# Performance work log

Measured on AMD Instinct MI355X. Metric: run time of the kernel, lower is better.

Reference implementation:

```python
import jax, jax.numpy as jnp
import numpy as np

B, C, H, W = 32, 512, 32, 32
HEADS = 8
HD = C // HEADS  # 64
BN_EPS = 1e-5


def setup_inputs() -> dict:
    key = jax.random.key(0)
    ks = jax.random.split(key, 8)
    s = 0.02  # trunc_normal std for Linear weights
    x = jax.random.normal(ks[0], (B, C, H, W), jnp.float32)
    Wq = jax.random.normal(ks[1], (C, C), jnp.float32) * s
    Wk = jax.random.normal(ks[2], (C, C), jnp.float32) * s
    Wv = jax.random.normal(ks[3], (C, C), jnp.float32) * s
    # depthwise 3x3 kernel, kaiming fan_out (fan_out = 3*3*1 per group)
    dw_w = jax.random.normal(ks[4], (C, 1, 3, 3), jnp.float32) * np.sqrt(2.0 / 9.0)
    bn_gamma = jnp.ones((C,), jnp.float32)
    bn_beta = jnp.zeros((C,), jnp.float32)
    temperature = jnp.ones((HEADS, 1, 1), jnp.float32)
    Wp = jax.random.normal(ks[5], (C, C), jnp.float32) * s
    bp = jnp.zeros((C,), jnp.float32)
    return {"x": x, "Wq": Wq, "Wk": Wk, "Wv": Wv, "dw_w": dw_w,
            "bn_gamma": bn_gamma, "bn_beta": bn_beta,
            "temperature": temperature, "Wp": Wp, "bp": bp}


def _l2norm(t):
    # torch F.normalize: x / max(||x||, eps)
    n = jnp.sqrt(jnp.sum(t * t, axis=-1, keepdims=True))
    return t / jnp.maximum(n, 1e-12)


def _forward(x, Wq, Wk, Wv, dw_w, bn_gamma, bn_beta, temperature, Wp, bp):
    b, c, h, w = x.shape
    n = h * w
    x_flat = x.transpose(0, 2, 3, 1).reshape(b, n, c)  # [B,N,C]

    q = (x_flat @ Wq.T).reshape(b, n, HEADS, HD).transpose(0, 2, 3, 1)  # [B,h,d,N]
    k = (x_flat @ Wk.T).reshape(b, n, HEADS, HD).transpose(0, 2, 3, 1)
    q = _l2norm(q)
    k = _l2norm(k)

    attn = jnp.einsum('bhdn,bhen->bhde', q, k) * temperature  # [B,h,d,d]
    attn = jax.nn.softmax(attn, axis=-1)

    v_content = x_flat @ Wv.T  # [B,N,C]

    # gated value path: DWConv -> BatchNorm (batch stats, train mode) -> SiLU
    g = jax.lax.conv_general_dilated(
        x, dw_w, window_strides=(1, 1), padding=((1, 1), (1, 1)),
        feature_group_count=c, dimension_numbers=('NCHW', 'OIHW', 'NCHW'))
    mu = jnp.mean(g, axis=(0, 2, 3), keepdims=True)
    var = jnp.var(g, axis=(0, 2, 3), keepdims=True)
    g = (g - mu) * jax.lax.rsqrt(var + BN_EPS)
    g = g * bn_gamma[None, :, None, None] + bn_beta[None, :, None, None]
    g = g * jax.nn.sigmoid(g)  # SiLU
    v_gate = g.transpose(0, 2, 3, 1).reshape(b, n, c)

    v = (v_content * v_gate).reshape(b, n, HEADS, HD).transpose(0, 2, 3, 1)  # [B,h,d,N]
    out = jnp.einsum('bhde,bhen->bhdn', attn, v)  # [B,h,d,N]
    out = out.transpose(0, 3, 1, 2).reshape(b, n, c)  # [B,N,C]
    out = out @ Wp.T + bp
    return out.reshape(b, h, w, c).transpose(0, 3, 1, 2)  # [B,C,H,W]


def reference(x, Wq, Wk, Wv, dw_w, bn_gamma, bn_beta, temperature, Wp, bp):
    return _forward(x, Wq, Wk, Wv, dw_w, bn_gamma, bn_beta, temperature, Wp, bp)
```

## Files before the change

kernel.cpp:

```cpp
#include <hip/hip_runtime.h>
#include <stdint.h>

#define BATCH 32
#define CCH   512
#define NPIX  1024
#define HEADS 8
#define QKV_M 1536

typedef short bf16x8 __attribute__((ext_vector_type(8)));
typedef float f32x4 __attribute__((ext_vector_type(4)));
typedef unsigned short u16x8 __attribute__((ext_vector_type(8)));

__device__ inline float bf2f(unsigned short u) {
  union { float f; uint32_t i; } t; t.i = ((uint32_t)u) << 16; return t.f;
}
__device__ inline unsigned short f2bf(float f) {
  union { float f; uint32_t u; } t; t.f = f;
  uint32_t u = t.u;
  return (unsigned short)((u + 0x7FFFu + ((u >> 16) & 1u)) >> 16);
}

__device__ inline void gl_lds16(const unsigned short* g, unsigned short* l) {
  __builtin_amdgcn_global_load_lds(
      (const __attribute__((address_space(1))) uint32_t*)g,
      (__attribute__((address_space(3))) uint32_t*)l, 16, 0, 0);
}

__global__ void convert_w(const float* __restrict__ Wq, const float* __restrict__ Wk,
                          const float* __restrict__ Wv, const float* __restrict__ Wp,
                          unsigned short* __restrict__ wcat,
                          unsigned short* __restrict__ wpb) {
  int i = (blockIdx.x * 256 + threadIdx.x) * 4;
  union { ushort4 u4; unsigned short s[4]; } o;
  f32x4 a;
  a = *(const f32x4*)&Wq[i];
  for (int j = 0; j < 4; j++) o.s[j] = f2bf(a[j]);
  *(ushort4*)&wcat[i] = o.u4;
  a = *(const f32x4*)&Wk[i];
  for (int j = 0; j < 4; j++) o.s[j] = f2bf(a[j]);
  *(ushort4*)&wcat[CCH * CCH + i] = o.u4;
  a = *(const f32x4*)&Wv[i];
  for (int j = 0; j < 4; j++) o.s[j] = f2bf(a[j]);
  *(ushort4*)&wcat[2 * CCH * CCH + i] = o.u4;
  a = *(const f32x4*)&Wp[i];
  for (int j = 0; j < 4; j++) o.s[j] = f2bf(a[j]);
  *(ushort4*)&wpb[i] = o.u4;
}

__global__ void transpose_f2b(const float* __restrict__ in,
                              unsigned short* __restrict__ out) {
  __shared__ float tile[64][65];
  const int b  = blockIdx.z;
  const int p0 = blockIdx.x * 64;
  const int c0 = blockIdx.y * 64;
  const float* inb = in + (size_t)b * CCH * NPIX;
  unsigned short* outb = out + (size_t)b * NPIX * CCH;
  const int t = threadIdx.x;
  const int cr = t >> 2, tl = t & 3;
#pragma unroll
  for (int j = 0; j < 4; ++j) {
    const int off = j * 16 + tl * 4;
    f32x4 v = *(const f32x4*)&inb[(size_t)(c0 + cr) * NPIX + p0 + off];
    tile[cr][off + 0] = v[0];
    tile[cr][off + 1] = v[1];
    tile[cr][off + 2] = v[2];
    tile[cr][off + 3] = v[3];
  }
  __syncthreads();
  const int pr = t >> 3, cc = (t & 7) * 8;
#pragma unroll
  for (int pass = 0; pass < 2; ++pass) {
    const int p = pr + pass * 32;
    union { u16x8 v; unsigned short s[8]; } o;
#pragma unroll
    for (int j = 0; j < 8; ++j) o.s[j] = f2bf(tile[cc + j][p]);
    *(u16x8*)&outb[(size_t)(p0 + p) * CCH + c0 + cc] = o.v;
  }
}

template <bool OUT_F32>
__launch_bounds__(512, 2)
__global__ void gemm_bt(const unsigned short* __restrict__ A,
                        const unsigned short* __restrict__ X,
                        void* __restrict__ Cout,
                        const float* __restrict__ bias,
                        int M, int N, int K) {
  __shared__ __align__(16) unsigned short As[2][256 * 64];
  __shared__ __align__(16) unsigned short Bs[2][256 * 64];
  const int b  = blockIdx.z;
  const int m0 = blockIdx.y * 256;
  const int n0 = blockIdx.x * 256;
  const unsigned short* Xb = X + (size_t)b * N * K;
  const int tid  = threadIdx.x;
  const int lane = tid & 63;
  const int wave = tid >> 6;
  const int wm = wave >> 2;
  const int wn = wave & 3;
  const int quad = lane >> 4, l16 = lane & 15;

  f32x4 acc[8][4];
  const f32x4 zero = {0.f, 0.f, 0.f, 0.f};
#pragma unroll
  for (int i = 0; i < 8; i++)
#pragma unroll
    for (int j = 0; j < 4; j++) acc[i][j] = zero;

  const int r8  = lane >> 3;
  const int swk = ((lane & 7) ^ r8) * 8;
  const unsigned short* Ag = A  + (size_t)(m0 + wave * 32 + r8) * K + swk;
  const unsigned short* Xg = Xb + (size_t)(n0 + wave * 32 + r8) * K + swk;

  const int NT = K >> 6;

  auto stage = [&](int kt, int bsel) {
    unsigned short* Al = &As[bsel][wave * 32 * 64];
    unsigned short* Bl = &Bs[bsel][wave * 32 * 64];
    const unsigned short* Agk = Ag + kt * 64;
    const unsigned short* Xgk = Xg + kt * 64;
#pragma unroll
    for (int i = 0; i < 4; ++i) {
      gl_lds16(Agk + (size_t)i * 8 * K, Al + i * 8 * 64);
      gl_lds16(Xgk + (size_t)i * 8 * K, Bl + i * 8 * 64);
    }
  };

  stage(0, 0);
  if (NT > 1) stage(1, 1);
  asm volatile("s_waitcnt vmcnt(8)" ::: "memory");
  __builtin_amdgcn_s_barrier();

  for (int t = 0; t < NT; ++t) {
    const int cur = t & 1;
    const unsigned short* Asl = As[cur];
    const unsigned short* Bsl = Bs[cur];

    {
      bf16x8 a0[8], b0[4];
      const int ch0 = ((0 * 4 + quad) ^ (l16 & 7)) * 8;
#pragma unroll
      for (int ii = 0; ii < 8; ++ii)
        a0[ii] = *(const bf16x8*)&Asl[(wm * 128 + ii * 16 + l16) * 64 + ch0];
#pragma unroll
      for (int jj = 0; jj < 4; ++jj)
        b0[jj] = *(const bf16x8*)&Bsl[(wn * 64 + jj * 16 + l16) * 64 + ch0];

      bf16x8 a1[8], b1[4];
      const int ch1 = ((1 * 4 + quad) ^ (l16 & 7)) * 8;
#pragma unroll
      for (int ii = 0; ii < 8; ++ii)
        a1[ii] = *(const bf16x8*)&Asl[(wm * 128 + ii * 16 + l16) * 64 + ch1];
#pragma unroll
      for (int jj = 0; jj < 4; ++jj)
        b1[jj] = *(const bf16x8*)&Bsl[(wn * 64 + jj * 16 + l16) * 64 + ch1];

#pragma unroll
      for (int ii = 0; ii < 8; ++ii)
#pragma unroll
        for (int jj = 0; jj < 4; ++jj)
          acc[ii][jj] = __builtin_amdgcn_mfma_f32_16x16x32_bf16(
              a0[ii], b0[jj], acc[ii][jj], 0, 0, 0);
#pragma unroll
      for (int ii = 0; ii < 8; ++ii)
#pragma unroll
        for (int jj = 0; jj < 4; ++jj)
          acc[ii][jj] = __builtin_amdgcn_mfma_f32_16x16x32_bf16(
              a1[ii], b1[jj], acc[ii][jj], 0, 0, 0);
    }

    __builtin_amdgcn_s_barrier();
    if (t + 2 < NT) {
      stage(t + 2, cur);
      asm volatile("s_waitcnt vmcnt(8)" ::: "memory");
    } else if (t + 1 < NT) {
      asm volatile("s_waitcnt vmcnt(0)" ::: "memory");
    }
    __builtin_amdgcn_s_barrier();
  }

#pragma unroll
  for (int i = 0; i < 8; ++i) {
#pragma unroll
    for (int r = 0; r < 4; ++r) {
      const int gm = m0 + wm * 128 + i * 16 + quad * 4 + r;
      if constexpr (OUT_F32) {
        const float bv = bias[gm];
        float* Co = (float*)Cout + (size_t)b * M * N + (size_t)gm * N +
                    n0 + wn * 64 + l16;
#pragma unroll
        for (int j = 0; j < 4; ++j) Co[j * 16] = acc[i][j][r] + bv;
      } else {
        unsigned short* Co = (unsigned short*)Cout + (size_t)b * M * N +
                             (size_t)gm * N + n0 + wn * 64 + l16;
#pragma unroll
        for (int j = 0; j < 4; ++j) Co[j * 16] = f2bf(acc[i][j][r]);
      }
    }
  }
}

__global__ void dw_stats(const float* __restrict__ x,
                         const float* __restrict__ wgt,
                         float* __restrict__ s1, float* __restrict__ s2) {
  int c = blockIdx.x, b = blockIdx.y;
  __shared__ __align__(16) float plane[NPIX];
  const float* xp = x + ((size_t)b * CCH + c) * NPIX;
  *(f32x4*)&plane[threadIdx.x * 4] = *(const f32x4*)&xp[threadIdx.x * 4];
  __syncthreads();
  float w[9];
  for (int i = 0; i < 9; i++) w[i] = wgt[c * 9 + i];
  float a1 = 0.f, a2 = 0.f;
  for (int pi = 0; pi < 4; pi++) {
    int p = threadIdx.x + pi * 256;
    int h = p >> 5, wc = p & 31;
    float v = 0.f;
    for (int dh = -1; dh <= 1; dh++)
      for (int dw = -1; dw <= 1; dw++) {
        int hh = h + dh, ww = wc + dw;
        if (hh >= 0 && hh < 32 && ww >= 0 && ww < 32)
          v += w[(dh + 1) * 3 + dw + 1] * plane[hh * 32 + ww];
      }
    a1 += v; a2 += v * v;
  }
  for (int off = 32; off > 0; off >>= 1) {
    a1 += __shfl_down(a1, off);
    a2 += __shfl_down(a2, off);
  }
  __shared__ float r1[4], r2[4];
  int wv = threadIdx.x >> 6;
  if ((threadIdx.x & 63) == 0) { r1[wv] = a1; r2[wv] = a2; }
  __syncthreads();
  if (threadIdx.x == 0) {
    atomicAdd(&s1[c], r1[0] + r1[1] + r1[2] + r1[3]);
    atomicAdd(&s2[c], r2[0] + r2[1] + r2[2] + r2[3]);
  }
}

__global__ void gate_apply(const float* __restrict__ x,
                           const float* __restrict__ wgt,
                           const float* __restrict__ s1, const float* __restrict__ s2,
                           const float* __restrict__ gamma,
                           const float* __restrict__ beta,
                           unsigned short* __restrict__ qkv) {
  int c = blockIdx.x, b = blockIdx.y;
  __shared__ __align__(16) float plane[NPIX];
  const float* xp = x + ((size_t)b * CCH + c) * NPIX;
  *(f32x4*)&plane[threadIdx.x * 4] = *(const f32x4*)&xp[threadIdx.x * 4];
  __syncthreads();
  float w[9];
  for (int i = 0; i < 9; i++) w[i] = wgt[c * 9 + i];
  const float invn = 1.f / 32768.f;
  float mean = s1[c] * invn;
  float var = fmaxf(s2[c] * invn - mean * mean, 0.f);
  float rstd = rsqrtf(var + 1e-5f);
  float ga = gamma[c], be = beta[c];

  const int t = threadIdx.x;
  const int h = t >> 3, w0 = (t & 7) * 4;
  unsigned short* vp = qkv + ((size_t)b * QKV_M + 2 * CCH + c) * NPIX + h * 32 + w0;
  union { ushort4 q; unsigned short s[4]; } vv;
  vv.q = *(const ushort4*)vp;
#pragma unroll
  for (int i = 0; i < 4; ++i) {
    const int wc = w0 + i;
    float val = 0.f;
    for (int dh = -1; dh <= 1; dh++)
      for (int dw = -1; dw <= 1; dw++) {
        int hh = h + dh, ww = wc + dw;
        if (hh >= 0 && hh < 32 && ww >= 0 && ww < 32)
          val += w[(dh + 1) * 3 + dw + 1] * plane[hh * 32 + ww];
      }
    float g = (val - mean) * rstd * ga + be;
    float sg = g / (1.f + __expf(-g));
    vv.s[i] = f2bf(bf2f(vv.s[i]) * sg);
  }
  *(ushort4*)vp = vv.q;
}

__launch_bounds__(256)
__global__ void attn_s(const unsigned short* __restrict__ qkv,
                       const float* __restrict__ temp,
                       unsigned short* __restrict__ P) {
  int bh = blockIdx.x;
  int b = bh >> 3, h = bh & 7;
  const unsigned short* Q = qkv + ((size_t)b * QKV_M + h * 64) * NPIX;
  const unsigned short* K = Q + (size_t)CCH * NPIX;
  int tid = threadIdx.x, lane = tid & 63, wave = tid >> 6;
  int quad = lane >> 4, l16 = lane & 15;

  __shared__ __align__(16) float Sf[64][65];
  __shared__ float qq[64], kk[64], invq[64], invk[64];
  __shared__ float redm[4][64], reds[4][64];

  f32x4 zero = {0.f, 0.f, 0.f, 0.f};
  f32x4 acc[4], accQ = zero, accK = zero;
  for (int j = 0; j < 4; j++) acc[j] = zero;
  for (int n0 = 0; n0 < NPIX; n0 += 32) {
    bf16x8 a  = *(const bf16x8*)&Q[(size_t)(wave * 16 + l16) * NPIX + n0 + quad * 8];
    bf16x8 ak = *(const bf16x8*)&K[(size_t)(wave * 16 + l16) * NPIX + n0 + quad * 8];
    accQ = __builtin_amdgcn_mfma_f32_16x16x32_bf16(a, a, accQ, 0, 0, 0);
    accK = __builtin_amdgcn_mfma_f32_16x16x32_bf16(ak, ak, accK, 0, 0, 0);
    for (int j = 0; j < 4; j++) {
      bf16x8 bb = *(const bf16x8*)&K[(size_t)(j * 16 + l16) * NPIX + n0 + quad * 8];
      acc[j] = __builtin_amdgcn_mfma_f32_16x16x32_bf16(a, bb, acc[j], 0, 0, 0);
    }
  }
  for (int j = 0; j < 4; j++)
    for (int r = 0; r < 4; r++)
      Sf[wave * 16 + quad * 4 + r][j * 16 + l16] = acc[j][r];
  for (int r = 0; r < 4; r++)
    if (l16 == quad * 4 + r) {
      qq[wave * 16 + l16] = accQ[r];
      kk[wave * 16 + l16] = accK[r];
    }
  __syncthreads();
  if (tid < 64) invq[tid] = 1.f / fmaxf(sqrtf(qq[tid]), 1e-12f);
  else if (tid < 128) invk[tid - 64] = 1.f / fmaxf(sqrtf(kk[tid - 64]), 1e-12f);
  __syncthreads();

  int row = tid & 63, seg = tid >> 6;
  float fq = temp[h] * invq[row];
  float v[16], pm = -1e30f;
  for (int i = 0; i < 16; i++) {
    v[i] = Sf[row][seg * 16 + i] * fq * invk[seg * 16 + i];
    pm = fmaxf(pm, v[i]);
  }
  redm[seg][row] = pm;
  __syncthreads();
  float m = fmaxf(fmaxf(redm[0][row], redm[1][row]),
                  fmaxf(redm[2][row], redm[3][row]));
  float ps = 0.f;
  for (int i = 0; i < 16; i++) { v[i] = __expf(v[i] - m); ps += v[i]; }
  reds[seg][row] = ps;
  __syncthreads();
  float inv = 1.f / (reds[0][row] + reds[1][row] + reds[2][row] + reds[3][row]);
  union { uint4 q4[2]; unsigned short s[16]; } u;
  for (int i = 0; i < 16; i++) u.s[i] = f2bf(v[i] * inv);
  unsigned short* Pp = P + ((size_t)bh * 64 + row) * 64 + seg * 16;
  *(uint4*)&Pp[0] = u.q4[0];
  *(uint4*)&Pp[8] = u.q4[1];
}

__launch_bounds__(256)
__global__ void attn_o(const unsigned short* __restrict__ qkv,
                       const unsigned short* __restrict__ P,
                       unsigned short* __restrict__ aoT) {
  int blk = blockIdx.x;
  int nc = blk & 3, bh = blk >> 2;
  int b = bh >> 3, h = bh & 7;
  const unsigned short* V = qkv + ((size_t)b * QKV_M + 2 * CCH + h * 64) * NPIX;
  unsigned short* Ob = aoT + (size_t)b * NPIX * CCH + h * 64;
  int tid = threadIdx.x, lane = tid & 63, wave = tid >> 6;
  int quad = lane >> 4, l16 = lane & 15;

  __shared__ __align__(16) unsigned short Vt[4][16][72];
  __shared__ __align__(16) unsigned short Ot[4][16][72];

  const unsigned short* Pb = P + (size_t)bh * 64 * 64;
  bf16x8 Pf[4][2];
  for (int j = 0; j < 4; j++)
    for (int ks = 0; ks < 2; ks++)
      Pf[j][ks] = *(const bf16x8*)&Pb[(j * 16 + l16) * 64 + ks * 32 + quad * 8];

  f32x4 zero = {0.f, 0.f, 0.f, 0.f};
  int e1 = lane >> 1, noff = (lane & 1) * 8;
  int nbase = nc * 256 + wave * 64;
  int orow = lane >> 3, ocol = (lane & 7) * 8;

  union { uint4 q; unsigned short s[8]; } g0, g1, c0, c1;
  g0.q = *(const uint4*)&V[(size_t)e1 * NPIX + nbase + noff];
  g1.q = *(const uint4*)&V[(size_t)(e1 + 32) * NPIX + nbase + noff];
#pragma unroll
  for (int nt = 0; nt < 4; nt++) {
    int n0 = nbase + nt * 16;
    c0 = g0; c1 = g1;
    if (nt < 3) {
      g0.q = *(const uint4*)&V[(size_t)e1 * NPIX + n0 + 16 + noff];
      g1.q = *(const uint4*)&V[(size_t)(e1 + 32) * NPIX + n0 + 16 + noff];
    }
    for (int jj = 0; jj < 8; jj++) {
      Vt[wave][noff + jj][e1]      = c0.s[jj];
      Vt[wave][noff + jj][e1 + 32] = c1.s[jj];
    }
    bf16x8 Af0 = *(const bf16x8*)&Vt[wave][l16][quad * 8];
    bf16x8 Af1 = *(const bf16x8*)&Vt[wave][l16][32 + quad * 8];
    f32x4 oacc[4];
    for (int j = 0; j < 4; j++) {
      oacc[j] = __builtin_amdgcn_mfma_f32_16x16x32_bf16(Af0, Pf[j][0], zero, 0, 0, 0);
      oacc[j] = __builtin_amdgcn_mfma_f32_16x16x32_bf16(Af1, Pf[j][1], oacc[j], 0, 0, 0);
    }
    for (int j = 0; j < 4; j++)
      for (int r = 0; r < 4; r++)
        Ot[wave][quad * 4 + r][j * 16 + l16] = f2bf(oacc[j][r]);
    uint4 o0 = *(const uint4*)&Ot[wave][orow][ocol];
    uint4 o1 = *(const uint4*)&Ot[wave][orow + 8][ocol];
    *(uint4*)&Ob[(size_t)(n0 + orow) * CCH + ocol] = o0;
    *(uint4*)&Ob[(size_t)(n0 + orow + 8) * CCH + ocol] = o1;
  }
}

extern "C" void kernel_launch(void* const* d_in, const int* in_sizes, int n_in,
                              void* d_out, int out_size, void* d_ws, size_t ws_size,
                              hipStream_t stream) {
  const float* x     = (const float*)d_in[0];
  const float* Wq    = (const float*)d_in[1];
  const float* Wk    = (const float*)d_in[2];
  const float* Wv    = (const float*)d_in[3];
  const float* dww   = (const float*)d_in[4];
  const float* gamma = (const float*)d_in[5];
  const float* beta  = (const float*)d_in[6];
  const float* temp  = (const float*)d_in[7];
  const float* Wp    = (const float*)d_in[8];
  const float* bp    = (const float*)d_in[9];
  float* out = (float*)d_out;

  char* ws = (char*)d_ws;
  unsigned short* wcat = (unsigned short*)ws;
  unsigned short* wpb  = wcat + (size_t)QKV_M * CCH;
  float* s1 = (float*)(wpb + (size_t)CCH * CCH);
  float* s2 = s1 + CCH;
  unsigned short* Pbuf = (unsigned short*)(s2 + CCH);
  char* dyn = (char*)(Pbuf + (size_t)BATCH * HEADS * 64 * 64);
  size_t fixed = (size_t)(dyn - ws);
  size_t per_b = ((size_t)NPIX * CCH + (size_t)QKV_M * NPIX) * 2;
  int BC = BATCH;
  while (BC > 1 && fixed + (size_t)BC * per_b > ws_size) BC >>= 1;
  unsigned short* xT  = (unsigned short*)dyn;
  unsigned short* qkv = xT + (size_t)BC * NPIX * CCH;

  convert_w<<<CCH * CCH / 1024, 256, 0, stream>>>(Wq, Wk, Wv, Wp, wcat, wpb);
  hipMemsetAsync(s1, 0, 2 * CCH * sizeof(float), stream);
  dw_stats<<<dim3(CCH, BATCH), 256, 0, stream>>>(x, dww, s1, s2);

  for (int b0 = 0; b0 < BATCH; b0 += BC) {
    const float* xc = x + (size_t)b0 * CCH * NPIX;
    float* outc = out + (size_t)b0 * CCH * NPIX;
    transpose_f2b<<<dim3(NPIX / 64, CCH / 64, BC), 256, 0, stream>>>(xc, xT);
    gemm_bt<false><<<dim3(NPIX / 256, QKV_M / 256, BC), 512, 0, stream>>>(
        wcat, xT, qkv, nullptr, QKV_M, NPIX, CCH);
    attn_s<<<BC * HEADS, 256, 0, stream>>>(qkv, temp, Pbuf);
    gate_apply<<<dim3(CCH, BC), 256, 0, stream>>>(xc, dww, s1, s2, gamma, beta, qkv);
    attn_o<<<BC * HEADS * 4, 256, 0, stream>>>(qkv, Pbuf, xT);
    gemm_bt<true><<<dim3(NPIX / 256, CCH / 256, BC), 512, 0, stream>>>(
        wpb, xT, outc, bp, CCH, NPIX, CCH);
  }
}
```

Before: 323.3 us.

## Split attention kernels across more waves and blocks for higher parallelism

attn_s now runs 16 waves per block, each handling a quarter of the pixel dimension. Partial Gram sums and squared norms are reduced through shared memory before the softmax, which is spread over 16 segments per row. attn_o launches twice as many blocks, each covering half the pixels. The aim is to raise occupancy: only 256 blocks of attn_s exist on a GPU with many CUs. The cost is a larger shared-memory footprint and an extra cross-wave reduction step.

```diff
diff --git a/kernel.cpp b/kernel.cpp
--- a/kernel.cpp
+++ b/kernel.cpp
@@ -276,7 +276,7 @@
   *(ushort4*)vp = vv.q;
 }
 
-__launch_bounds__(256)
+__launch_bounds__(1024)
 __global__ void attn_s(const unsigned short* __restrict__ qkv,
                        const float* __restrict__ temp,
                        unsigned short* __restrict__ P) {
@@ -285,59 +285,88 @@
   const unsigned short* Q = qkv + ((size_t)b * QKV_M + h * 64) * NPIX;
   const unsigned short* K = Q + (size_t)CCH * NPIX;
   int tid = threadIdx.x, lane = tid & 63, wave = tid >> 6;
+  int r16 = wave & 3;
+  int ns  = wave >> 2;
   int quad = lane >> 4, l16 = lane & 15;
 
-  __shared__ __align__(16) float Sf[64][65];
-  __shared__ float qq[64], kk[64], invq[64], invk[64];
-  __shared__ float redm[4][64], reds[4][64];
+  __shared__ float Sp[4][64][68];
+  __shared__ float qqp[4][64], kkp[4][64];
+  __shared__ float invq[64], invk[64];
+  __shared__ float redm[16][64], reds[16][64];
 
   f32x4 zero = {0.f, 0.f, 0.f, 0.f};
   f32x4 acc[4], accQ = zero, accK = zero;
+#pragma unroll
   for (int j = 0; j < 4; j++) acc[j] = zero;
-  for (int n0 = 0; n0 < NPIX; n0 += 32) {
-    bf16x8 a  = *(const bf16x8*)&Q[(size_t)(wave * 16 + l16) * NPIX + n0 + quad * 8];
-    bf16x8 ak = *(const bf16x8*)&K[(size_t)(wave * 16 + l16) * NPIX + n0 + quad * 8];
+
+  const int nbase = ns * 256;
+  for (int n0 = nbase; n0 < nbase + 256; n0 += 32) {
+    bf16x8 a  = *(const bf16x8*)&Q[(size_t)(r16 * 16 + l16) * NPIX + n0 + quad * 8];
+    bf16x8 ak = *(const bf16x8*)&K[(size_t)(r16 * 16 + l16) * NPIX + n0 + quad * 8];
     accQ = __builtin_amdgcn_mfma_f32_16x16x32_bf16(a, a, accQ, 0, 0, 0);
     accK = __builtin_amdgcn_mfma_f32_16x16x32_bf16(ak, ak, accK, 0, 0, 0);
+#pragma unroll
     for (int j = 0; j < 4; j++) {
       bf16x8 bb = *(const bf16x8*)&K[(size_t)(j * 16 + l16) * NPIX + n0 + quad * 8];
       acc[j] = __builtin_amdgcn_mfma_f32_16x16x32_bf16(a, bb, acc[j], 0, 0, 0);
     }
   }
+#pragma unroll
   for (int j = 0; j < 4; j++)
+#pragma unroll
     for (int r = 0; r < 4; r++)
-      Sf[wave * 16 + quad * 4 + r][j * 16 + l16] = acc[j][r];
+      Sp[ns][r16 * 16 + quad * 4 + r][j * 16 + l16] = acc[j][r];
+#pragma unroll
   for (int r = 0; r < 4; r++)
     if (l16 == quad * 4 + r) {
-      qq[wave * 16 + l16] = accQ[r];
-      kk[wave * 16 + l16] = accK[r];
-    }
-  __syncthreads();
-  if (tid < 64) invq[tid] = 1.f / fmaxf(sqrtf(qq[tid]), 1e-12f);
-  else if (tid < 128) invk[tid - 64] = 1.f / fmaxf(sqrtf(kk[tid - 64]), 1e-12f);
-  __syncthreads();
-
-  int row = tid & 63, seg = tid >> 6;
+      qqp[ns][r16 * 16 + l16] = accQ[r];
+      kkp[ns][r16 * 16 + l16] = accK[r];
+    }
+  __syncthreads();
+
+  const int row = tid >> 4, c0 = (tid & 15) * 4;
+#pragma unroll
+  for (int i = 0; i < 4; ++i) {
+    float s = Sp[0][row][c0 + i] + Sp[1][row][c0 + i] +
+              Sp[2][row][c0 + i] + Sp[3][row][c0 + i];
+    Sp[0][row][c0 + i] = s;
+  }
+  if (tid < 64) {
+    float q4 = qqp[0][tid] + qqp[1][tid] + qqp[2][tid] + qqp[3][tid];
+    invq[tid] = 1.f / fmaxf(sqrtf(q4), 1e-12f);
+  } else if (tid < 128) {
+    int r = tid - 64;
+    float k4 = kkp[0][r] + kkp[1][r] + kkp[2][r] + kkp[3][r];
+    invk[r] = 1.f / fmaxf(sqrtf(k4), 1e-12f);
+  }
+  __syncthreads();
+
+  const int seg = tid & 15;
   float fq = temp[h] * invq[row];
-  float v[16], pm = -1e30f;
-  for (int i = 0; i < 16; i++) {
-    v[i] = Sf[row][seg * 16 + i] * fq * invk[seg * 16 + i];
+  float v[4], pm = -1e30f;
+#pragma unroll
+  for (int i = 0; i < 4; i++) {
+    v[i] = Sp[0][row][seg * 4 + i] * fq * invk[seg * 4 + i];
     pm = fmaxf(pm, v[i]);
   }
   redm[seg][row] = pm;
   __syncthreads();
-  float m = fmaxf(fmaxf(redm[0][row], redm[1][row]),
-                  fmaxf(redm[2][row], redm[3][row]));
+  float m = -1e30f;
+#pragma unroll
+  for (int s = 0; s < 16; s++) m = fmaxf(m, redm[s][row]);
   float ps = 0.f;
-  for (int i = 0; i < 16; i++) { v[i] = __expf(v[i] - m); ps += v[i]; }
+#pragma unroll
+  for (int i = 0; i < 4; i++) { v[i] = __expf(v[i] - m); ps += v[i]; }
   reds[seg][row] = ps;
   __syncthreads();
-  float inv = 1.f / (reds[0][row] + reds[1][row] + reds[2][row] + reds[3][row]);
-  union { uint4 q4[2]; unsigned short s[16]; } u;
-  for (int i = 0; i < 16; i++) u.s[i] = f2bf(v[i] * inv);
-  unsigned short* Pp = P + ((size_t)bh * 64 + row) * 64 + seg * 16;
-  *(uint4*)&Pp[0] = u.q4[0];
-  *(uint4*)&Pp[8] = u.q4[1];
+  float tot = 0.f;
+#pragma unroll
+  for (int s = 0; s < 16; s++) tot += reds[s][row];
+  float inv = 1.f / tot;
+  union { ushort4 q; unsigned short s[4]; } u;
+#pragma unroll
+  for (int i = 0; i < 4; i++) u.s[i] = f2bf(v[i] * inv);
+  *(ushort4*)&P[((size_t)bh * 64 + row) * 64 + seg * 4] = u.q;
 }
 
 __launch_bounds__(256)
@@ -345,7 +374,7 @@
                        const unsigned short* __restrict__ P,
                        unsigned short* __restrict__ aoT) {
   int blk = blockIdx.x;
-  int nc = blk & 3, bh = blk >> 2;
+  int nc = blk & 7, bh = blk >> 3;
   int b = bh >> 3, h = bh & 7;
   const unsigned short* V = qkv + ((size_t)b * QKV_M + 2 * CCH + h * 64) * NPIX;
   unsigned short* Ob = aoT + (size_t)b * NPIX * CCH + h * 64;
@@ -363,17 +392,17 @@
 
   f32x4 zero = {0.f, 0.f, 0.f, 0.f};
   int e1 = lane >> 1, noff = (lane & 1) * 8;
-  int nbase = nc * 256 + wave * 64;
+  int nbase = nc * 128 + wave * 32;
   int orow = lane >> 3, ocol = (lane & 7) * 8;
 
   union { uint4 q; unsigned short s[8]; } g0, g1, c0, c1;
   g0.q = *(const uint4*)&V[(size_t)e1 * NPIX + nbase + noff];
   g1.q = *(const uint4*)&V[(size_t)(e1 + 32) * NPIX + nbase + noff];
 #pragma unroll
-  for (int nt = 0; nt < 4; nt++) {
+  for (int nt = 0; nt < 2; nt++) {
     int n0 = nbase + nt * 16;
     c0 = g0; c1 = g1;
-    if (nt < 3) {
+    if (nt < 1) {
       g0.q = *(const uint4*)&V[(size_t)e1 * NPIX + n0 + 16 + noff];
       g1.q = *(const uint4*)&V[(size_t)(e1 + 32) * NPIX + n0 + 16 + noff];
     }
@@ -437,9 +466,9 @@
     transpose_f2b<<<dim3(NPIX / 64, CCH / 64, BC), 256, 0, stream>>>(xc, xT);
     gemm_bt<false><<<dim3(NPIX / 256, QKV_M / 256, BC), 512, 0, stream>>>(
         wcat, xT, qkv, nullptr, QKV_M, NPIX, CCH);
-    attn_s<<<BC * HEADS, 256, 0, stream>>>(qkv, temp, Pbuf);
+    attn_s<<<BC * HEADS, 1024, 0, stream>>>(qkv, temp, Pbuf);
     gate_apply<<<dim3(CCH, BC), 256, 0, stream>>>(xc, dww, s1, s2, gamma, beta, qkv);
-    attn_o<<<BC * HEADS * 4, 256, 0, stream>>>(qkv, Pbuf, xT);
+    attn_o<<<BC * HEADS * 8, 256, 0, stream>>>(qkv, Pbuf, xT);
     gemm_bt<true><<<dim3(NPIX / 256, CCH / 256, BC), 512, 0, stream>>>(
         wpb, xT, outc, bp, CCH, NPIX, CCH);
   }
```

Measured after the change: 322.9 us. Within noise of the previous version (-0.1%).

## Merge independent kernels into combined launches and split attn_o finer

Applied to the files above, without the earlier changes.

Folds the stats zeroing into the weight-conversion kernel, replacing hipMemsetAsync. Merges dw_stats with the input transpose, and gate_apply with attn_s, as block-index-dispatched combined kernels so independent work shares a launch and fills the GPU. It also doubles attn_o's grid with half the pixel range per block. The fast path applies only when the whole batch fits in workspace. The legacy chunked path is kept as a fallback, at the cost of more LDS per merged block and mixed workloads in one grid.

```diff
diff --git a/kernel.cpp b/kernel.cpp
--- a/kernel.cpp
+++ b/kernel.cpp
@@ -26,10 +26,16 @@
       (__attribute__((address_space(3))) uint32_t*)l, 16, 0, 0);
 }
 
-__global__ void convert_w(const float* __restrict__ Wq, const float* __restrict__ Wk,
-                          const float* __restrict__ Wv, const float* __restrict__ Wp,
-                          unsigned short* __restrict__ wcat,
-                          unsigned short* __restrict__ wpb) {
+__global__ void prep_w(const float* __restrict__ Wq, const float* __restrict__ Wk,
+                       const float* __restrict__ Wv, const float* __restrict__ Wp,
+                       unsigned short* __restrict__ wcat,
+                       unsigned short* __restrict__ wpb,
+                       float* __restrict__ s1, float* __restrict__ s2) {
+  if (blockIdx.x == 0) {
+    const f32x4 z4 = {0.f, 0.f, 0.f, 0.f};
+    if (threadIdx.x < 128) ((f32x4*)s1)[threadIdx.x] = z4;
+    else ((f32x4*)s2)[threadIdx.x - 128] = z4;
+  }
   int i = (blockIdx.x * 256 + threadIdx.x) * 4;
   union { ushort4 u4; unsigned short s[4]; } o;
   f32x4 a;
@@ -47,14 +53,48 @@
   *(ushort4*)&wpb[i] = o.u4;
 }
 
-__global__ void transpose_f2b(const float* __restrict__ in,
-                              unsigned short* __restrict__ out) {
-  __shared__ float tile[64][65];
-  const int b  = blockIdx.z;
-  const int p0 = blockIdx.x * 64;
-  const int c0 = blockIdx.y * 64;
-  const float* inb = in + (size_t)b * CCH * NPIX;
-  unsigned short* outb = out + (size_t)b * NPIX * CCH;
+
+__device__ __forceinline__ void stats_body(const float* __restrict__ xp,
+                                           const float* __restrict__ wgt, int c,
+                                           float* __restrict__ s1,
+                                           float* __restrict__ s2,
+                                           float* __restrict__ plane,
+                                           float* __restrict__ r1,
+                                           float* __restrict__ r2) {
+  *(f32x4*)&plane[threadIdx.x * 4] = *(const f32x4*)&xp[threadIdx.x * 4];
+  __syncthreads();
+  float w[9];
+  for (int i = 0; i < 9; i++) w[i] = wgt[c * 9 + i];
+  float a1 = 0.f, a2 = 0.f;
+  for (int pi = 0; pi < 4; pi++) {
+    int p = threadIdx.x + pi * 256;
+    int h = p >> 5, wc = p & 31;
+    float v = 0.f;
+    for (int dh = -1; dh <= 1; dh++)
+      for (int dw = -1; dw <= 1; dw++) {
+        int hh = h + dh, ww = wc + dw;
+        if (hh >= 0 && hh < 32 && ww >= 0 && ww < 32)
+          v += w[(dh + 1) * 3 + dw + 1] * plane[hh * 32 + ww];
+      }
+    a1 += v; a2 += v * v;
+  }
+  for (int off = 32; off > 0; off >>= 1) {
+    a1 += __shfl_down(a1, off);
+    a2 += __shfl_down(a2, off);
+  }
+  int wv = threadIdx.x >> 6;
+  if ((threadIdx.x & 63) == 0) { r1[wv] = a1; r2[wv] = a2; }
+  __syncthreads();
+  if (threadIdx.x == 0) {
+    atomicAdd(&s1[c], r1[0] + r1[1] + r1[2] + r1[3]);
+    atomicAdd(&s2[c], r2[0] + r2[1] + r2[2] + r2[3]);
+  }
+}
+
+__device__ __forceinline__ void transpose_body(const float* __restrict__ inb,
+                                               unsigned short* __restrict__ outb,
+                                               int p0, int c0,
+                                               float (*tile)[65]) {
   const int t = threadIdx.x;
   const int cr = t >> 2, tl = t & 3;
 #pragma unroll
@@ -76,6 +116,186 @@
     for (int j = 0; j < 8; ++j) o.s[j] = f2bf(tile[cc + j][p]);
     *(u16x8*)&outb[(size_t)(p0 + p) * CCH + c0 + cc] = o.v;
   }
+}
+
+__device__ __forceinline__ void gate_body(const float* __restrict__ xp,
+                                          const float* __restrict__ wgt, int c,
+                                          const float* __restrict__ s1,
+                                          const float* __restrict__ s2,
+                                          const float* __restrict__ gamma,
+                                          const float* __restrict__ beta,
+                                          unsigned short* __restrict__ vbase,
+                                          float* __restrict__ plane) {
+  *(f32x4*)&plane[threadIdx.x * 4] = *(const f32x4*)&xp[threadIdx.x * 4];
+  __syncthreads();
+  float w[9];
+  for (int i = 0; i < 9; i++) w[i] = wgt[c * 9 + i];
+  const float invn = 1.f / 32768.f;
+  float mean = s1[c] * invn;
+  float var = fmaxf(s2[c] * invn - mean * mean, 0.f);
+  float rstd = rsqrtf(var + 1e-5f);
+  float ga = gamma[c], be = beta[c];
+  const int t = threadIdx.x;
+  const int h = t >> 3, w0 = (t & 7) * 4;
+  unsigned short* vp = vbase + h * 32 + w0;
+  union { ushort4 q; unsigned short s[4]; } vv;
+  vv.q = *(const ushort4*)vp;
+#pragma unroll
+  for (int i = 0; i < 4; ++i) {
+    const int wc = w0 + i;
+    float val = 0.f;
+    for (int dh = -1; dh <= 1; dh++)
+      for (int dw = -1; dw <= 1; dw++) {
+        int hh = h + dh, ww = wc + dw;
+        if (hh >= 0 && hh < 32 && ww >= 0 && ww < 32)
+          val += w[(dh + 1) * 3 + dw + 1] * plane[hh * 32 + ww];
+      }
+    float g = (val - mean) * rstd * ga + be;
+    float sg = g / (1.f + __expf(-g));
+    vv.s[i] = f2bf(bf2f(vv.s[i]) * sg);
+  }
+  *(ushort4*)vp = vv.q;
+}
+
+__device__ __forceinline__ void attn_s_body(const unsigned short* __restrict__ qkv,
+                                            const float* __restrict__ temp,
+                                            unsigned short* __restrict__ P, int bh,
+                                            float (*Sf)[65],
+                                            float* qq, float* kk,
+                                            float* invq, float* invk,
+                                            float (*redm)[64], float (*reds)[64]) {
+  int b = bh >> 3, h = bh & 7;
+  const unsigned short* Q = qkv + ((size_t)b * QKV_M + h * 64) * NPIX;
+  const unsigned short* K = Q + (size_t)CCH * NPIX;
+  int tid = threadIdx.x, lane = tid & 63, wave = tid >> 6;
+  int quad = lane >> 4, l16 = lane & 15;
+
+  f32x4 zero = {0.f, 0.f, 0.f, 0.f};
+  f32x4 acc[4], accQ = zero, accK = zero;
+  for (int j = 0; j < 4; j++) acc[j] = zero;
+  for (int n0 = 0; n0 < NPIX; n0 += 32) {
+    bf16x8 a  = *(const bf16x8*)&Q[(size_t)(wave * 16 + l16) * NPIX + n0 + quad * 8];
+    bf16x8 ak = *(const bf16x8*)&K[(size_t)(wave * 16 + l16) * NPIX + n0 + quad * 8];
+    accQ = __builtin_amdgcn_mfma_f32_16x16x32_bf16(a, a, accQ, 0, 0, 0);
+    accK = __builtin_amdgcn_mfma_f32_16x16x32_bf16(ak, ak, accK, 0, 0, 0);
+    for (int j = 0; j < 4; j++) {
+      bf16x8 bb = *(const bf16x8*)&K[(size_t)(j * 16 + l16) * NPIX + n0 + quad * 8];
+      acc[j] = __builtin_amdgcn_mfma_f32_16x16x32_bf16(a, bb, acc[j], 0, 0, 0);
+    }
+  }
+  for (int j = 0; j < 4; j++)
+    for (int r = 0; r < 4; r++)
+      Sf[wave * 16 + quad * 4 + r][j * 16 + l16] = acc[j][r];
+  for (int r = 0; r < 4; r++)
+    if (l16 == quad * 4 + r) {
+      qq[wave * 16 + l16] = accQ[r];
+      kk[wave * 16 + l16] = accK[r];
+    }
+  __syncthreads();
+  if (tid < 64) invq[tid] = 1.f / fmaxf(sqrtf(qq[tid]), 1e-12f);
+  else if (tid < 128) invk[tid - 64] = 1.f / fmaxf(sqrtf(kk[tid - 64]), 1e-12f);
+  __syncthreads();
+
+  int row = tid & 63, seg = tid >> 6;
+  float fq = temp[h] * invq[row];
+  float v[16], pm = -1e30f;
+  for (int i = 0; i < 16; i++) {
+    v[i] = Sf[row][seg * 16 + i] * fq * invk[seg * 16 + i];
+    pm = fmaxf(pm, v[i]);
+  }
+  redm[seg][row] = pm;
+  __syncthreads();
+  float m = fmaxf(fmaxf(redm[0][row], redm[1][row]),
+                  fmaxf(redm[2][row], redm[3][row]));
+  float ps = 0.f;
+  for (int i = 0; i < 16; i++) { v[i] = __expf(v[i] - m); ps += v[i]; }
+  reds[seg][row] = ps;
+  __syncthreads();
+  float inv = 1.f / (reds[0][row] + reds[1][row] + reds[2][row] + reds[3][row]);
+  union { uint4 q4[2]; unsigned short s[16]; } u;
+  for (int i = 0; i < 16; i++) u.s[i] = f2bf(v[i] * inv);
+  unsigned short* Pp = P + ((size_t)bh * 64 + row) * 64 + seg * 16;
+  *(uint4*)&Pp[0] = u.q4[0];
+  *(uint4*)&Pp[8] = u.q4[1];
+}
+
+__global__ void stats_transpose(const float* __restrict__ x,
+                                const float* __restrict__ wgt,
+                                float* __restrict__ s1, float* __restrict__ s2,
+                                unsigned short* __restrict__ xT) {
+  __shared__ float tile[64][65];
+  __shared__ float r1[4], r2[4];
+  const int bid = blockIdx.x;
+  if (bid < CCH * BATCH) {
+    const int c = bid & (CCH - 1), b = bid >> 9;
+    stats_body(x + ((size_t)b * CCH + c) * NPIX, wgt, c, s1, s2,
+               &tile[0][0], r1, r2);
+  } else {
+    const int j = bid - CCH * BATCH;
+    const int p0 = (j & 15) * 64, c0 = ((j >> 4) & 7) * 64, b = j >> 7;
+    transpose_body(x + (size_t)b * CCH * NPIX, xT + (size_t)b * NPIX * CCH,
+                   p0, c0, tile);
+  }
+}
+
+__global__ void attn_gate(unsigned short* __restrict__ qkv,
+                          const float* __restrict__ temp,
+                          unsigned short* __restrict__ P,
+                          const float* __restrict__ x,
+                          const float* __restrict__ wgt,
+                          const float* __restrict__ s1,
+                          const float* __restrict__ s2,
+                          const float* __restrict__ gamma,
+                          const float* __restrict__ beta) {
+  __shared__ float Sf[64][65];
+  __shared__ float qq[64], kk[64], invq[64], invk[64];
+  __shared__ float redm[4][64], reds[4][64];
+  const int bid = blockIdx.x;
+  if (bid < CCH * BATCH) {
+    const int c = bid & (CCH - 1), b = bid >> 9;
+    gate_body(x + ((size_t)b * CCH + c) * NPIX, wgt, c, s1, s2, gamma, beta,
+              qkv + ((size_t)b * QKV_M + 2 * CCH + c) * NPIX, &Sf[0][0]);
+  } else {
+    attn_s_body(qkv, temp, P, bid - CCH * BATCH,
+                Sf, qq, kk, invq, invk, redm, reds);
+  }
+}
+
+__global__ void transpose_f2b(const float* __restrict__ in,
+                              unsigned short* __restrict__ out) {
+  __shared__ float tile[64][65];
+  transpose_body(in + (size_t)blockIdx.z * CCH * NPIX,
+                 out + (size_t)blockIdx.z * NPIX * CCH,
+                 blockIdx.x * 64, blockIdx.y * 64, tile);
+}
+
+__global__ void dw_stats(const float* __restrict__ x, const float* __restrict__ wgt,
+                         float* __restrict__ s1, float* __restrict__ s2) {
+  __shared__ float plane[NPIX];
+  __shared__ float r1[4], r2[4];
+  int c = blockIdx.x, b = blockIdx.y;
+  stats_body(x + ((size_t)b * CCH + c) * NPIX, wgt, c, s1, s2, plane, r1, r2);
+}
+
+__global__ void gate_apply(const float* __restrict__ x, const float* __restrict__ wgt,
+                           const float* __restrict__ s1, const float* __restrict__ s2,
+                           const float* __restrict__ gamma,
+                           const float* __restrict__ beta,
+                           unsigned short* __restrict__ qkv) {
+  __shared__ float plane[NPIX];
+  int c = blockIdx.x, b = blockIdx.y;
+  gate_body(x + ((size_t)b * CCH + c) * NPIX, wgt, c, s1, s2, gamma, beta,
+            qkv + ((size_t)b * QKV_M + 2 * CCH + c) * NPIX, plane);
+}
+
+__launch_bounds__(256)
+__global__ void attn_s(const unsigned short* __restrict__ qkv,
+                       const float* __restrict__ temp,
+                       unsigned short* __restrict__ P) {
+  __shared__ float Sf[64][65];
+  __shared__ float qq[64], kk[64], invq[64], invk[64];
+  __shared__ float redm[4][64], reds[4][64];
+  attn_s_body(qkv, temp, P, blockIdx.x, Sf, qq, kk, invq, invk, redm, reds);
 }
 
 template <bool OUT_F32>
@@ -198,154 +418,12 @@
   }
 }
 
-__global__ void dw_stats(const float* __restrict__ x,
-                         const float* __restrict__ wgt,
-                         float* __restrict__ s1, float* __restrict__ s2) {
-  int c = blockIdx.x, b = blockIdx.y;
-  __shared__ __align__(16) float plane[NPIX];
-  const float* xp = x + ((size_t)b * CCH + c) * NPIX;
-  *(f32x4*)&plane[threadIdx.x * 4] = *(const f32x4*)&xp[threadIdx.x * 4];
-  __syncthreads();
-  float w[9];
-  for (int i = 0; i < 9; i++) w[i] = wgt[c * 9 + i];
-  float a1 = 0.f, a2 = 0.f;
-  for (int pi = 0; pi < 4; pi++) {
-    int p = threadIdx.x + pi * 256;
-    int h = p >> 5, wc = p & 31;
-    float v = 0.f;
-    for (int dh = -1; dh <= 1; dh++)
-      for (int dw = -1; dw <= 1; dw++) {
-        int hh = h + dh, ww = wc + dw;
-        if (hh >= 0 && hh < 32 && ww >= 0 && ww < 32)
-          v += w[(dh + 1) * 3 + dw + 1] * plane[hh * 32 + ww];
-      }
-    a1 += v; a2 += v * v;
-  }
-  for (int off = 32; off > 0; off >>= 1) {
-    a1 += __shfl_down(a1, off);
-    a2 += __shfl_down(a2, off);
-  }
-  __shared__ float r1[4], r2[4];
-  int wv = threadIdx.x >> 6;
-  if ((threadIdx.x & 63) == 0) { r1[wv] = a1; r2[wv] = a2; }
-  __syncthreads();
-  if (threadIdx.x == 0) {
-    atomicAdd(&s1[c], r1[0] + r1[1] + r1[2] + r1[3]);
-    atomicAdd(&s2[c], r2[0] + r2[1] + r2[2] + r2[3]);
-  }
-}
-
-__global__ void gate_apply(const float* __restrict__ x,
-                           const float* __restrict__ wgt,
-                           const float* __restrict__ s1, const float* __restrict__ s2,
-                           const float* __restrict__ gamma,
-                           const float* __restrict__ beta,
-                           unsigned short* __restrict__ qkv) {
-  int c = blockIdx.x, b = blockIdx.y;
-  __shared__ __align__(16) float plane[NPIX];
-  const float* xp = x + ((size_t)b * CCH + c) * NPIX;
-  *(f32x4*)&plane[threadIdx.x * 4] = *(const f32x4*)&xp[threadIdx.x * 4];
-  __syncthreads();
-  float w[9];
-  for (int i = 0; i < 9; i++) w[i] = wgt[c * 9 + i];
-  const float invn = 1.f / 32768.f;
-  float mean = s1[c] * invn;
-  float var = fmaxf(s2[c] * invn - mean * mean, 0.f);
-  float rstd = rsqrtf(var + 1e-5f);
-  float ga = gamma[c], be = beta[c];
-
-  const int t = threadIdx.x;
-  const int h = t >> 3, w0 = (t & 7) * 4;
-  unsigned short* vp = qkv + ((size_t)b * QKV_M + 2 * CCH + c) * NPIX + h * 32 + w0;
-  union { ushort4 q; unsigned short s[4]; } vv;
-  vv.q = *(const ushort4*)vp;
-#pragma unroll
-  for (int i = 0; i < 4; ++i) {
-    const int wc = w0 + i;
-    float val = 0.f;
-    for (int dh = -1; dh <= 1; dh++)
-      for (int dw = -1; dw <= 1; dw++) {
-        int hh = h + dh, ww = wc + dw;
-        if (hh >= 0 && hh < 32 && ww >= 0 && ww < 32)
-          val += w[(dh + 1) * 3 + dw + 1] * plane[hh * 32 + ww];
-      }
-    float g = (val - mean) * rstd * ga + be;
-    float sg = g / (1.f + __expf(-g));
-    vv.s[i] = f2bf(bf2f(vv.s[i]) * sg);
-  }
-  *(ushort4*)vp = vv.q;
-}
-
-__launch_bounds__(256)
-__global__ void attn_s(const unsigned short* __restrict__ qkv,
-                       const float* __restrict__ temp,
-                       unsigned short* __restrict__ P) {
-  int bh = blockIdx.x;
-  int b = bh >> 3, h = bh & 7;
-  const unsigned short* Q = qkv + ((size_t)b * QKV_M + h * 64) * NPIX;
-  const unsigned short* K = Q + (size_t)CCH * NPIX;
-  int tid = threadIdx.x, lane = tid & 63, wave = tid >> 6;
-  int quad = lane >> 4, l16 = lane & 15;
-
-  __shared__ __align__(16) float Sf[64][65];
-  __shared__ float qq[64], kk[64], invq[64], invk[64];
-  __shared__ float redm[4][64], reds[4][64];
-
-  f32x4 zero = {0.f, 0.f, 0.f, 0.f};
-  f32x4 acc[4], accQ = zero, accK = zero;
-  for (int j = 0; j < 4; j++) acc[j] = zero;
-  for (int n0 = 0; n0 < NPIX; n0 += 32) {
-    bf16x8 a  = *(const bf16x8*)&Q[(size_t)(wave * 16 + l16) * NPIX + n0 + quad * 8];
-    bf16x8 ak = *(const bf16x8*)&K[(size_t)(wave * 16 + l16) * NPIX + n0 + quad * 8];
-    accQ = __builtin_amdgcn_mfma_f32_16x16x32_bf16(a, a, accQ, 0, 0, 0);
-    accK = __builtin_amdgcn_mfma_f32_16x16x32_bf16(ak, ak, accK, 0, 0, 0);
-    for (int j = 0; j < 4; j++) {
-      bf16x8 bb = *(const bf16x8*)&K[(size_t)(j * 16 + l16) * NPIX + n0 + quad * 8];
-      acc[j] = __builtin_amdgcn_mfma_f32_16x16x32_bf16(a, bb, acc[j], 0, 0, 0);
-    }
-  }
-  for (int j = 0; j < 4; j++)
-    for (int r = 0; r < 4; r++)
-      Sf[wave * 16 + quad * 4 + r][j * 16 + l16] = acc[j][r];
-  for (int r = 0; r < 4; r++)
-    if (l16 == quad * 4 + r) {
-      qq[wave * 16 + l16] = accQ[r];
-      kk[wave * 16 + l16] = accK[r];
-    }
-  __syncthreads();
-  if (tid < 64) invq[tid] = 1.f / fmaxf(sqrtf(qq[tid]), 1e-12f);
-  else if (tid < 128) invk[tid - 64] = 1.f / fmaxf(sqrtf(kk[tid - 64]), 1e-12f);
-  __syncthreads();
-
-  int row = tid & 63, seg = tid >> 6;
-  float fq = temp[h] * invq[row];
-  float v[16], pm = -1e30f;
-  for (int i = 0; i < 16; i++) {
-    v[i] = Sf[row][seg * 16 + i] * fq * invk[seg * 16 + i];
-    pm = fmaxf(pm, v[i]);
-  }
-  redm[seg][row] = pm;
-  __syncthreads();
-  float m = fmaxf(fmaxf(redm[0][row], redm[1][row]),
-                  fmaxf(redm[2][row], redm[3][row]));
-  float ps = 0.f;
-  for (int i = 0; i < 16; i++) { v[i] = __expf(v[i] - m); ps += v[i]; }
-  reds[seg][row] = ps;
-  __syncthreads();
-  float inv = 1.f / (reds[0][row] + reds[1][row] + reds[2][row] + reds[3][row]);
-  union { uint4 q4[2]; unsigned short s[16]; } u;
-  for (int i = 0; i < 16; i++) u.s[i] = f2bf(v[i] * inv);
-  unsigned short* Pp = P + ((size_t)bh * 64 + row) * 64 + seg * 16;
-  *(uint4*)&Pp[0] = u.q4[0];
-  *(uint4*)&Pp[8] = u.q4[1];
-}
-
 __launch_bounds__(256)
 __global__ void attn_o(const unsigned short* __restrict__ qkv,
                        const unsigned short* __restrict__ P,
                        unsigned short* __restrict__ aoT) {
   int blk = blockIdx.x;
-  int nc = blk & 3, bh = blk >> 2;
+  int nc = blk & 7, bh = blk >> 3;
   int b = bh >> 3, h = bh & 7;
   const unsigned short* V = qkv + ((size_t)b * QKV_M + 2 * CCH + h * 64) * NPIX;
   unsigned short* Ob = aoT + (size_t)b * NPIX * CCH + h * 64;
@@ -363,17 +441,17 @@
 
   f32x4 zero = {0.f, 0.f, 0.f, 0.f};
   int e1 = lane >> 1, noff = (lane & 1) * 8;
-  int nbase = nc * 256 + wave * 64;
+  int nbase = nc * 128 + wave * 32;
   int orow = lane >> 3, ocol = (lane & 7) * 8;
 
   union { uint4 q; unsigned short s[8]; } g0, g1, c0, c1;
   g0.q = *(const uint4*)&V[(size_t)e1 * NPIX + nbase + noff];
   g1.q = *(const uint4*)&V[(size_t)(e1 + 32) * NPIX + nbase + noff];
 #pragma unroll
-  for (int nt = 0; nt < 4; nt++) {
+  for (int nt = 0; nt < 2; nt++) {
     int n0 = nbase + nt * 16;
     c0 = g0; c1 = g1;
-    if (nt < 3) {
+    if (nt < 1) {
       g0.q = *(const uint4*)&V[(size_t)e1 * NPIX + n0 + 16 + noff];
       g1.q = *(const uint4*)&V[(size_t)(e1 + 32) * NPIX + n0 + 16 + noff];
     }
@@ -427,20 +505,31 @@
   unsigned short* xT  = (unsigned short*)dyn;
   unsigned short* qkv = xT + (size_t)BC * NPIX * CCH;
 
-  convert_w<<<CCH * CCH / 1024, 256, 0, stream>>>(Wq, Wk, Wv, Wp, wcat, wpb);
-  hipMemsetAsync(s1, 0, 2 * CCH * sizeof(float), stream);
-  dw_stats<<<dim3(CCH, BATCH), 256, 0, stream>>>(x, dww, s1, s2);
-
-  for (int b0 = 0; b0 < BATCH; b0 += BC) {
-    const float* xc = x + (size_t)b0 * CCH * NPIX;
-    float* outc = out + (size_t)b0 * CCH * NPIX;
-    transpose_f2b<<<dim3(NPIX / 64, CCH / 64, BC), 256, 0, stream>>>(xc, xT);
-    gemm_bt<false><<<dim3(NPIX / 256, QKV_M / 256, BC), 512, 0, stream>>>(
+  prep_w<<<CCH * CCH / 1024, 256, 0, stream>>>(Wq, Wk, Wv, Wp, wcat, wpb, s1, s2);
+
+  if (BC == BATCH) {
+    stats_transpose<<<CCH * BATCH + (NPIX / 64) * (CCH / 64) * BATCH, 256, 0,
+                      stream>>>(x, dww, s1, s2, xT);
+    gemm_bt<false><<<dim3(NPIX / 256, QKV_M / 256, BATCH), 512, 0, stream>>>(
         wcat, xT, qkv, nullptr, QKV_M, NPIX, CCH);
-    attn_s<<<BC * HEADS, 256, 0, stream>>>(qkv, temp, Pbuf);
-    gate_apply<<<dim3(CCH, BC), 256, 0, stream>>>(xc, dww, s1, s2, gamma, beta, qkv);
-    attn_o<<<BC * HEADS * 4, 256, 0, stream>>>(qkv, Pbuf, xT);
-    gemm_bt<true><<<dim3(NPIX / 256, CCH / 256, BC), 512, 0, stream>>>(
-        wpb, xT, outc, bp, CCH, NPIX, CCH);
-  }
-}
+    attn_gate<<<CCH * BATCH + BATCH * HEADS, 256, 0, stream>>>(
+        qkv, temp, Pbuf, x, dww, s1, s2, gamma, beta);
+    attn_o<<<BATCH * HEADS * 8, 256, 0, stream>>>(qkv, Pbuf, xT);
+    gemm_bt<true><<<dim3(NPIX / 256, CCH / 256, BATCH), 512, 0, stream>>>(
+        wpb, xT, out, bp, CCH, NPIX, CCH);
+  } else {
+    dw_stats<<<dim3(CCH, BATCH), 256, 0, stream>>>(x, dww, s1, s2);
+    for (int b0 = 0; b0 < BATCH; b0 += BC) {
+      const float* xc = x + (size_t)b0 * CCH * NPIX;
+      float* outc = out + (size_t)b0 * CCH * NPIX;
+      transpose_f2b<<<dim3(NPIX / 64, CCH / 64, BC), 256, 0, stream>>>(xc, xT);
+      gemm_bt<false><<<dim3(NPIX / 256, QKV_M / 256, BC), 512, 0, stream>>>(
+          wcat, xT, qkv, nullptr, QKV_M, NPIX, CCH);
+      attn_s<<<BC * HEADS, 256, 0, stream>>>(qkv, temp, Pbuf);
+      gate_apply<<<dim3(CCH, BC), 256, 0, stream>>>(xc, dww, s1, s2, gamma, beta, qkv);
+      attn_o<<<BC * HEADS * 8, 256, 0, stream>>>(qkv, Pbuf, xT);
+      gemm_bt<true><<<dim3(NPIX / 256, CCH / 256, BC), 512, 0, stream>>>(
+          wpb, xT, outc, bp, CCH, NPIX, CCH);
+    }
+  }
+}
```

Result: slower. 343.5 us (+6.3%).
